# Performance work log

Measured on AMD Instinct MI355X. Metric: run time of the kernel, lower is better.

Reference implementation:

```python
import jax, jax.numpy as jnp
import numpy as np

N_NODES = 100000
N_EDGES = 1000000
N_GRAPHS = 64
NODE_IN = 4
HID = 64
SIG = 16
NEG_SLOPE = 0.2


def _gat_layer(x, src, dst, W, a_src, a_dst, bias, n_nodes, concat):
    # W: [H*D, F_in], a_src/a_dst: [H, D], bias: [H*D] or [D]
    H, D = a_src.shape
    h = (x @ W.T).reshape(-1, H, D)                      # [N, H, D]
    alpha_src = jnp.sum(h * a_src[None], axis=-1)        # [N, H]
    alpha_dst = jnp.sum(h * a_dst[None], axis=-1)        # [N, H]
    e = alpha_src[src] + alpha_dst[dst]                  # [E, H]
    e = jax.nn.leaky_relu(e, NEG_SLOPE)
    # segment softmax over edges grouped by destination node
    e_max = jax.ops.segment_max(e, dst, num_segments=n_nodes)   # [N, H]
    e_exp = jnp.exp(e - e_max[dst])                              # [E, H]
    denom = jax.ops.segment_sum(e_exp, dst, num_segments=n_nodes)
    alpha = e_exp / denom[dst]                                   # [E, H]
    out = jax.ops.segment_sum(alpha[:, :, None] * h[src], dst, num_segments=n_nodes)  # [N,H,D]
    if concat:
        out = out.reshape(-1, H * D)
    else:
        out = out.mean(axis=1)
    return out + bias


def setup_inputs() -> dict:
    key = jax.random.key(0)
    ks = jax.random.split(key, 16)
    x = jax.random.normal(ks[0], (N_NODES, NODE_IN), dtype=jnp.float32)
    edge_index = jax.random.randint(ks[1], (2, N_EDGES), 0, N_NODES, dtype=jnp.int32)
    batch = jnp.sort(jax.random.randint(ks[2], (N_NODES,), 0, N_GRAPHS, dtype=jnp.int32))
    s = 0.1
    # conv1: heads=2, concat -> out 128
    w1 = jax.random.normal(ks[3], (2 * HID, NODE_IN), dtype=jnp.float32) * s
    att_src1 = jax.random.normal(ks[4], (2, HID), dtype=jnp.float32) * s
    att_dst1 = jax.random.normal(ks[5], (2, HID), dtype=jnp.float32) * s
    b1 = jnp.zeros((2 * HID,), dtype=jnp.float32)
    # conv2: heads=1, mean -> out 64
    w2 = jax.random.normal(ks[6], (HID, 2 * HID), dtype=jnp.float32) * s
    att_src2 = jax.random.normal(ks[7], (1, HID), dtype=jnp.float32) * s
    att_dst2 = jax.random.normal(ks[8], (1, HID), dtype=jnp.float32) * s
    b2 = jnp.zeros((HID,), dtype=jnp.float32)
    wp = jax.random.normal(ks[9], (SIG, HID), dtype=jnp.float32) * s
    bp = jnp.zeros((SIG,), dtype=jnp.float32)
    return {"x": x, "edge_index": edge_index, "batch": batch,
            "w1": w1, "att_src1": att_src1, "att_dst1": att_dst1, "b1": b1,
            "w2": w2, "att_src2": att_src2, "att_dst2": att_dst2, "b2": b2,
            "wp": wp, "bp": bp}


def reference(x, edge_index, batch, w1, att_src1, att_dst1, b1,
              w2, att_src2, att_dst2, b2, wp, bp):
    n = x.shape[0]
    loops = jnp.arange(n, dtype=edge_index.dtype)
    src = jnp.concatenate([edge_index[0], loops])  # PyG GATConv adds self-loops
    dst = jnp.concatenate([edge_index[1], loops])
    h = jax.nn.elu(_gat_layer(x, src, dst, w1, att_src1, att_dst1, b1, n, concat=True))
    h = jax.nn.elu(_gat_layer(h, src, dst, w2, att_src2, att_dst2, b2, n, concat=False))
    # global mean pool by graph id
    sums = jax.ops.segment_sum(h, batch, num_segments=N_GRAPHS)
    cnts = jax.ops.segment_sum(jnp.ones((n,), h.dtype), batch, num_segments=N_GRAPHS)
    pooled = sums / jnp.maximum(cnts, 1.0)[:, None]
    return (pooled @ wp.T + bp).squeeze()
```

## Files before the change

### kernel.cpp

```cpp
#include <hip/hip_runtime.h>
#include <hip/hip_fp16.h>

#define N_NODES  100000
#define N_EDGES  1000000
#define E_TOT    1100000
#define E_CAP    1900000
#define N_GRAPHS 64

typedef _Float16 half8 __attribute__((ext_vector_type(8)));
typedef float    f32x4 __attribute__((ext_vector_type(4)));

__device__ __forceinline__ float elu_f(float v) {
    return v > 0.f ? v : expm1f(v);
}

__device__ __forceinline__ float lrelu(float v) {
    return v > 0.f ? v : 0.2f * v;
}

__global__ void k_pre(const float* __restrict__ w1,
                      const float* __restrict__ as1v, const float* __restrict__ ad1v,
                      const float* __restrict__ w2,
                      const float* __restrict__ as2v, const float* __restrict__ ad2v,
                      float* __restrict__ A1, float* __restrict__ D1,
                      float* __restrict__ B2, float* __restrict__ E2)
{
    int t = threadIdx.x;
    if (t < 128) {
        float acc = 0.f;
        for (int d = 0; d < 64; ++d) acc += w2[d * 128 + t] * as2v[d];
        B2[t] = acc;
    } else {
        int k = t - 128;
        float acc = 0.f;
        for (int d = 0; d < 64; ++d) acc += w2[d * 128 + k] * ad2v[d];
        E2[k] = acc;
    }
    if (t < 8) {
        int h = t >> 2, k = t & 3;
        float acc = 0.f;
        for (int d = 0; d < 64; ++d) acc += w1[(h * 64 + d) * 4 + k] * as1v[h * 64 + d];
        A1[t] = acc;
    } else if (t < 16) {
        int i = t - 8, h = i >> 2, k = i & 3;
        float acc = 0.f;
        for (int d = 0; d < 64; ++d) acc += w1[(h * 64 + d) * 4 + k] * ad1v[h * 64 + d];
        D1[i] = acc;
    }
}

__global__ void k_pre2(const float* __restrict__ w2, __half* __restrict__ w2frag)
{
    int f = blockIdx.x * 256 + threadIdx.x;
    int j = f & 7, ln = (f >> 3) & 63, g = f >> 9;
    int nt = g >> 2, ks = g & 3;
    int col = nt * 16 + (ln & 15);
    int k   = ks * 32 + ((ln >> 4) << 3) + j;
    w2frag[f] = __float2half(w2[col * 128 + k]);
}

__global__ void k_count(const int* __restrict__ ei, int* __restrict__ deg, int* __restrict__ pos)
{
    int e = blockIdx.x * blockDim.x + threadIdx.x;
    if (e >= E_TOT) return;
    int dst = (e < N_EDGES) ? ei[N_EDGES + e] : (e - N_EDGES);
    pos[e] = atomicAdd(&deg[dst], 1);
}

__global__ void k_scan1(const int* __restrict__ deg, int* __restrict__ rowptr, int* __restrict__ bsum)
{
    __shared__ int sh[256];
    int tid = threadIdx.x;
    int i = blockIdx.x * 256 + tid;
    int v = (i <= N_NODES) ? ((deg[i] + 7) & ~7) : 0;
    int acc = v;
    sh[tid] = acc; __syncthreads();
    for (int off = 1; off < 256; off <<= 1) {
        int add = (tid >= off) ? sh[tid - off] : 0;
        __syncthreads();
        acc += add;
        sh[tid] = acc;
        __syncthreads();
    }
    if (i <= N_NODES) rowptr[i] = acc - v;
    if (tid == 255) bsum[blockIdx.x] = acc;
}

__global__ void k_scan2(int* __restrict__ bsum, int nb)
{
    __shared__ int sh[512];
    int tid = threadIdx.x;
    int v = (tid < nb) ? bsum[tid] : 0;
    int acc = v;
    sh[tid] = acc; __syncthreads();
    for (int off = 1; off < 512; off <<= 1) {
        int add = (tid >= off) ? sh[tid - off] : 0;
        __syncthreads();
        acc += add;
        sh[tid] = acc;
        __syncthreads();
    }
    if (tid < nb) bsum[tid] = acc - v;
}

__global__ void k_scan3(int* __restrict__ rowptr, const int* __restrict__ bsum)
{
    int i = blockIdx.x * 256 + threadIdx.x;
    if (i <= N_NODES) rowptr[i] += bsum[blockIdx.x];
}

__global__ void k_scatter(const int* __restrict__ ei, const int* __restrict__ rowptr,
                          const int* __restrict__ pos, int* __restrict__ srcs)
{
    int e = blockIdx.x * blockDim.x + threadIdx.x;
    if (e >= E_TOT) return;
    int src = (e < N_EDGES) ? ei[e] : (e - N_EDGES);
    int dst = (e < N_EDGES) ? ei[N_EDGES + e] : (e - N_EDGES);
    srcs[rowptr[dst] + pos[e]] = src;
}

__global__ void __launch_bounds__(256) k_gather1x(
    const int* __restrict__ srcs, const int* __restrict__ rowptr, const int* __restrict__ deg,
    const float* __restrict__ x,
    const float* __restrict__ A1c, const float* __restrict__ D1c,
    float4* __restrict__ agg0, float4* __restrict__ agg1, float2* __restrict__ wsA)
{
    const int tid  = threadIdx.x;
    const int n    = blockIdx.x * 16 + (tid >> 4);
    const int lane = tid & 15;
    if (n >= N_NODES) return;

    const float4 A0 = ((const float4*)A1c)[0], A1v = ((const float4*)A1c)[1];
    const float4 D0 = ((const float4*)D1c)[0], D1v = ((const float4*)D1c)[1];
    const float4 xn = ((const float4*)x)[n];
    const float ad0 = xn.x * D0.x + xn.y * D0.y + xn.z * D0.z + xn.w * D0.w;
    const float ad1 = xn.x * D1v.x + xn.y * D1v.y + xn.z * D1v.z + xn.w * D1v.w;

    const int beg = rowptr[n], rend = beg + deg[n];
    float4 acc0 = {0.f, 0.f, 0.f, 0.f}, acc1 = {0.f, 0.f, 0.f, 0.f};
    float ws0 = 0.f, ws1 = 0.f;
    for (int j = beg + lane; j < rend; j += 16) {
        const int s = srcs[j];
        const float4 xs = ((const float4*)x)[s];
        const float as0 = xs.x * A0.x + xs.y * A0.y + xs.z * A0.z + xs.w * A0.w;
        const float as1 = xs.x * A1v.x + xs.y * A1v.y + xs.z * A1v.z + xs.w * A1v.w;
        const float w0 = __expf(lrelu(as0 + ad0));
        const float w1 = __expf(lrelu(as1 + ad1));
        acc0.x = fmaf(w0, xs.x, acc0.x); acc0.y = fmaf(w0, xs.y, acc0.y);
        acc0.z = fmaf(w0, xs.z, acc0.z); acc0.w = fmaf(w0, xs.w, acc0.w);
        acc1.x = fmaf(w1, xs.x, acc1.x); acc1.y = fmaf(w1, xs.y, acc1.y);
        acc1.z = fmaf(w1, xs.z, acc1.z); acc1.w = fmaf(w1, xs.w, acc1.w);
        ws0 += w0; ws1 += w1;
    }
    #pragma unroll
    for (int off = 1; off < 16; off <<= 1) {
        acc0.x += __shfl_xor(acc0.x, off, 64);
        acc0.y += __shfl_xor(acc0.y, off, 64);
        acc0.z += __shfl_xor(acc0.z, off, 64);
        acc0.w += __shfl_xor(acc0.w, off, 64);
        acc1.x += __shfl_xor(acc1.x, off, 64);
        acc1.y += __shfl_xor(acc1.y, off, 64);
        acc1.z += __shfl_xor(acc1.z, off, 64);
        acc1.w += __shfl_xor(acc1.w, off, 64);
        ws0    += __shfl_xor(ws0,    off, 64);
        ws1    += __shfl_xor(ws1,    off, 64);
    }
    if (lane == 0) {
        agg0[n] = acc0;
        agg1[n] = acc1;
        wsA[n]  = make_float2(ws0, ws1);
    }
}

#define H2_NPB 64
#define SROW_H_LD 136
__global__ void __launch_bounds__(256) k_h2f(
    const float4* __restrict__ agg0, const float4* __restrict__ agg1,
    const float2* __restrict__ wsA,
    const float* __restrict__ w1, const float* __restrict__ b1,
    const __half* __restrict__ w2frag,
    const float* __restrict__ B2, const float* __restrict__ E2,
    __half* __restrict__ h2h, float* __restrict__ as2, float* __restrict__ ad2)
{
    __shared__ __align__(16) _Float16 srow[H2_NPB * SROW_H_LD];
    const int tid = threadIdx.x;
    const int bn  = blockIdx.x * H2_NPB;

    #pragma unroll 4
    for (int t = 0; t < 16; ++t) {
        int i = tid + t * 256;
        int r = i >> 6, c2 = i & 63;
        int n = bn + r;
        int head = c2 >> 5;
        float4 a; float ws;
        if (n < N_NODES) {
            a = head ? agg1[n] : agg0[n];
            float2 w = wsA[n];
            ws = head ? w.y : w.x;
        } else { a = make_float4(0.f, 0.f, 0.f, 0.f); ws = 1.f; }
        const float4 wA = ((const float4*)w1)[2 * c2];
        const float4 wB = ((const float4*)w1)[2 * c2 + 1];
        const float2 bb = ((const float2*)b1)[c2];
        float inv = 1.f / ws;
        float v0 = elu_f((a.x * wA.x + a.y * wA.y + a.z * wA.z + a.w * wA.w) * inv + bb.x);
        float v1 = elu_f((a.x * wB.x + a.y * wB.y + a.z * wB.z + a.w * wB.w) * inv + bb.y);
        *(__half2*)&srow[r * SROW_H_LD + 2 * c2] = __floats2half2_rn(v0, v1);
    }
    __syncthreads();

    {
        int r = tid >> 2, q = tid & 3;
        const __half2* row = (const __half2*)&srow[r * SROW_H_LD];
        float ps = 0.f, pd = 0.f;
        #pragma unroll 4
        for (int i = 0; i < 16; ++i) {
            int c2 = q * 16 + i;
            float2 v  = __half22float2(row[c2]);
            float2 Bv = ((const float2*)B2)[c2];
            float2 Ev = ((const float2*)E2)[c2];
            ps += v.x * Bv.x + v.y * Bv.y;
            pd += v.x * Ev.x + v.y * Ev.y;
        }
        ps += __shfl_xor(ps, 1, 64); ps += __shfl_xor(ps, 2, 64);
        pd += __shfl_xor(pd, 1, 64); pd += __shfl_xor(pd, 2, 64);
        int n = bn + r;
        if (q == 0 && n < N_NODES) { as2[n] = ps; ad2[n] = pd; }
    }

    const int lane = tid & 63;
    const int wv   = tid >> 6;
    const int mrow = lane & 15;
    const int kc   = lane >> 4;
    f32x4 acc[4] = {{0.f,0.f,0.f,0.f},{0.f,0.f,0.f,0.f},{0.f,0.f,0.f,0.f},{0.f,0.f,0.f,0.f}};
    const half8* __restrict__ wf = (const half8*)w2frag;
    #pragma unroll
    for (int ks = 0; ks < 4; ++ks) {
        const half8 af = *(const half8*)&srow[(wv * 16 + mrow) * SROW_H_LD + ks * 32 + kc * 8];
        #pragma unroll
        for (int nt = 0; nt < 4; ++nt) {
            const half8 bf = wf[(nt * 4 + ks) * 64 + lane];
            acc[nt] = __builtin_amdgcn_mfma_f32_16x16x32_f16(af, bf, acc[nt], 0, 0, 0);
        }
    }
    #pragma unroll
    for (int nt = 0; nt < 4; ++nt) {
        #pragma unroll
        for (int reg = 0; reg < 4; ++reg) {
            int node = bn + wv * 16 + ((lane >> 4) << 2) + reg;
            int dim  = nt * 16 + (lane & 15);
            if (node < N_NODES) h2h[(size_t)node * 64 + dim] = __float2half(acc[nt][reg]);
        }
    }
}

__global__ void __launch_bounds__(256) k_weights2(
    const int* __restrict__ rowptr, const int* __restrict__ deg, int* __restrict__ srcs,
    const float* __restrict__ as2, const float* __restrict__ ad2,
    float* __restrict__ w0p)
{
    int n = blockIdx.x * 16 + (threadIdx.x >> 4);
    int lane = threadIdx.x & 15;
    if (n >= N_NODES) return;
    int beg = rowptr[n], pend = rowptr[n + 1], rend = beg + deg[n];
    float adv = ad2[n];
    for (int j = beg + lane; j < pend; j += 16) {
        if (j < rend) {
            w0p[j] = __expf(lrelu(as2[srcs[j]] + adv));
        } else {
            srcs[j] = 0;
            w0p[j] = 0.f;
        }
    }
}

__global__ void __launch_bounds__(256) k_gather2(
    const int* __restrict__ srcs, const int* __restrict__ rowptr,
    const float* __restrict__ wcsr, const _Float16* __restrict__ h2h,
    const float* __restrict__ b2, float* __restrict__ out2)
{
    const int tid  = threadIdx.x;
    const int n    = blockIdx.x * 4 + (tid >> 6);
    const int lane = tid & 63;
    const int eg   = lane >> 3;
    const int dq   = lane & 7;
    const int beg = rowptr[n], end = rowptr[n + 1];

    half8 hacc = {0, 0, 0, 0, 0, 0, 0, 0};
    float wsum = 0.f;
    for (int j = beg + eg; j < end; j += 8) {
        const int   s = srcs[j];
        const float w = wcsr[j];
        const half8 v = *(const half8*)&h2h[(size_t)s * 64 + dq * 8];
        const _Float16 wh = (_Float16)w;
        const half8 ws8 = {wh, wh, wh, wh, wh, wh, wh, wh};
        hacc += v * ws8;
        wsum += w;
    }
    float a0 = (float)hacc[0], a1 = (float)hacc[1], a2 = (float)hacc[2], a3 = (float)hacc[3];
    float a4 = (float)hacc[4], a5 = (float)hacc[5], a6 = (float)hacc[6], a7 = (float)hacc[7];
    #pragma unroll
    for (int off = 8; off < 64; off <<= 1) {
        a0 += __shfl_xor(a0, off, 64);
        a1 += __shfl_xor(a1, off, 64);
        a2 += __shfl_xor(a2, off, 64);
        a3 += __shfl_xor(a3, off, 64);
        a4 += __shfl_xor(a4, off, 64);
        a5 += __shfl_xor(a5, off, 64);
        a6 += __shfl_xor(a6, off, 64);
        a7 += __shfl_xor(a7, off, 64);
        wsum += __shfl_xor(wsum, off, 64);
    }
    if (eg == 0) {
        const float inv = 1.f / wsum;
        const float4 bA = ((const float4*)b2)[dq * 2];
        const float4 bB = ((const float4*)b2)[dq * 2 + 1];
        float4 oA, oB;
        oA.x = elu_f(a0 * inv + bA.x);
        oA.y = elu_f(a1 * inv + bA.y);
        oA.z = elu_f(a2 * inv + bA.z);
        oA.w = elu_f(a3 * inv + bA.w);
        oB.x = elu_f(a4 * inv + bB.x);
        oB.y = elu_f(a5 * inv + bB.y);
        oB.z = elu_f(a6 * inv + bB.z);
        oB.w = elu_f(a7 * inv + bB.w);
        float4* orow = (float4*)(out2 + (size_t)n * 64);
        orow[dq * 2]     = oA;
        orow[dq * 2 + 1] = oB;
    }
}

__global__ void __launch_bounds__(256) k_pool(
    const float* __restrict__ out2, const int* __restrict__ batch,
    float* __restrict__ pool, float* __restrict__ cnt)
{
    const int wv = threadIdx.x >> 6, d = threadIdx.x & 63;
    const int wid = blockIdx.x * 4 + wv;
    const int per = (N_NODES + 2047) / 2048;
    int n0 = wid * per, n1 = min(n0 + per, N_NODES);
    if (n0 >= n1) return;
    float acc = 0.f; int g = batch[n0]; int run = 0;
    for (int n = n0; n < n1; ++n) {
        int gn = batch[n];
        if (gn != g) {
            atomicAdd(&pool[g * 64 + d], acc);
            if (d == 0) atomicAdd(&cnt[g], (float)run);
            acc = 0.f; run = 0; g = gn;
        }
        acc += out2[(size_t)n * 64 + d];
        ++run;
    }
    atomicAdd(&pool[g * 64 + d], acc);
    if (d == 0) atomicAdd(&cnt[g], (float)run);
}

__global__ void k_head(const float* __restrict__ pool, const float* __restrict__ cnt,
                       const float* __restrict__ wp, const float* __restrict__ bp,
                       float* __restrict__ out)
{
    int t = threadIdx.x;
    int g = t >> 4, s = t & 15;
    float c = cnt[g]; if (c < 1.f) c = 1.f;
    float acc = bp[s];
    for (int d = 0; d < 64; ++d) acc += (pool[g * 64 + d] / c) * wp[s * 64 + d];
    out[g * 16 + s] = acc;
}

extern "C" void kernel_launch(void* const* d_in, const int* in_sizes, int n_in,
                              void* d_out, int out_size, void* d_ws, size_t ws_size,
                              hipStream_t stream)
{
    const float* x     = (const float*)d_in[0];
    const int*   ei    = (const int*)  d_in[1];
    const int*   batch = (const int*)  d_in[2];
    const float* w1    = (const float*)d_in[3];
    const float* asr1  = (const float*)d_in[4];
    const float* adr1  = (const float*)d_in[5];
    const float* b1    = (const float*)d_in[6];
    const float* w2    = (const float*)d_in[7];
    const float* asr2  = (const float*)d_in[8];
    const float* adr2  = (const float*)d_in[9];
    const float* b2    = (const float*)d_in[10];
    const float* wp    = (const float*)d_in[11];
    const float* bp    = (const float*)d_in[12];
    float* out = (float*)d_out;

    float4* agg0 = (float4*)d_ws;
    float4* agg1 = agg0 + N_NODES;
    float2* wsA  = (float2*)(agg1 + N_NODES);
    __half* h2h  = (__half*)(wsA + N_NODES);
    float* out2  = (float*)(h2h + (size_t)N_NODES * 64);
    float* as2   = out2 + (size_t)N_NODES * 64;
    float* ad2   = as2 + N_NODES;
    float* pool  = ad2 + N_NODES;
    float* cnt   = pool + N_GRAPHS * 64;
    int* deg     = (int*)(cnt + N_GRAPHS);
    int* rowptr  = deg + N_NODES + 1;
    int* pos     = rowptr + N_NODES + 1;
    int* srcs    = pos + E_TOT;
    float* wcsr  = (float*)(srcs + E_CAP);
    int* bsum    = (int*)(wcsr + E_CAP);
    float* A1    = (float*)(bsum + 512);
    float* D1    = A1 + 8;
    float* B2    = D1 + 8;
    float* E2    = B2 + 128;
    __half* w2frag = (__half*)(((uintptr_t)(E2 + 128) + 15) & ~(uintptr_t)15);

    hipMemsetAsync(deg, 0, (size_t)(N_NODES + 1) * sizeof(int), stream);
    hipMemsetAsync(pool, 0, (size_t)(N_GRAPHS * 64 + N_GRAPHS) * sizeof(float), stream);

    k_pre<<<1, 256, 0, stream>>>(w1, asr1, adr1, w2, asr2, adr2, A1, D1, B2, E2);
    k_pre2<<<32, 256, 0, stream>>>(w2, w2frag);

    const int eb  = (E_TOT + 255) / 256;
    const int nb1 = (N_NODES + 1 + 255) / 256;
    k_count<<<eb, 256, 0, stream>>>(ei, deg, pos);
    k_scan1<<<nb1, 256, 0, stream>>>(deg, rowptr, bsum);
    k_scan2<<<1, 512, 0, stream>>>(bsum, nb1);
    k_scan3<<<nb1, 256, 0, stream>>>(rowptr, bsum);
    k_scatter<<<eb, 256, 0, stream>>>(ei, rowptr, pos, srcs);

    const int gb = (N_NODES + 15) / 16;
    k_gather1x<<<gb, 256, 0, stream>>>(srcs, rowptr, deg, x, A1, D1, agg0, agg1, wsA);

    k_h2f<<<(N_NODES + H2_NPB - 1) / H2_NPB, 256, 0, stream>>>(
        agg0, agg1, wsA, w1, b1, w2frag, B2, E2, h2h, as2, ad2);

    k_weights2<<<gb, 256, 0, stream>>>(rowptr, deg, srcs, as2, ad2, wcsr);
    k_gather2<<<N_NODES / 4, 256, 0, stream>>>(srcs, rowptr, wcsr, (const _Float16*)h2h,
                                               b2, out2);

    k_pool<<<512, 256, 0, stream>>>(out2, batch, pool, cnt);
    k_head<<<1, 1024, 0, stream>>>(pool, cnt, wp, bp, out);
}
```

Before: 230.7 us.

## Merge precompute kernels, scatter via atomic cursor, split gather2 launch

Merges the two weight-precompute kernels into one 33-block launch. CSR construction no longer writes a per-edge position array in the count pass; the scan fills a per-node cursor and the scatter claims slots with atomics, which saves a 1.1M-int write and read but adds a second atomic pass and makes edge order within a row nondeterministic. The second-layer gather is split into two half-size launches over node ranges, which adds a launch without any evident benefit.

```diff
diff --git a/kernel.cpp b/kernel.cpp
--- a/kernel.cpp
+++ b/kernel.cpp
@@ -18,53 +18,53 @@
     return v > 0.f ? v : 0.2f * v;
 }
 
-__global__ void k_pre(const float* __restrict__ w1,
-                      const float* __restrict__ as1v, const float* __restrict__ ad1v,
-                      const float* __restrict__ w2,
-                      const float* __restrict__ as2v, const float* __restrict__ ad2v,
-                      float* __restrict__ A1, float* __restrict__ D1,
-                      float* __restrict__ B2, float* __restrict__ E2)
-{
-    int t = threadIdx.x;
-    if (t < 128) {
-        float acc = 0.f;
-        for (int d = 0; d < 64; ++d) acc += w2[d * 128 + t] * as2v[d];
-        B2[t] = acc;
+__global__ void k_preall(const float* __restrict__ w1,
+                         const float* __restrict__ as1v, const float* __restrict__ ad1v,
+                         const float* __restrict__ w2,
+                         const float* __restrict__ as2v, const float* __restrict__ ad2v,
+                         float* __restrict__ A1, float* __restrict__ D1,
+                         float* __restrict__ B2, float* __restrict__ E2,
+                         __half* __restrict__ w2frag)
+{
+    if (blockIdx.x == 0) {
+        int t = threadIdx.x;
+        if (t < 128) {
+            float acc = 0.f;
+            for (int d = 0; d < 64; ++d) acc += w2[d * 128 + t] * as2v[d];
+            B2[t] = acc;
+        } else {
+            int k = t - 128;
+            float acc = 0.f;
+            for (int d = 0; d < 64; ++d) acc += w2[d * 128 + k] * ad2v[d];
+            E2[k] = acc;
+        }
+        if (t < 8) {
+            int h = t >> 2, k = t & 3;
+            float acc = 0.f;
+            for (int d = 0; d < 64; ++d) acc += w1[(h * 64 + d) * 4 + k] * as1v[h * 64 + d];
+            A1[t] = acc;
+        } else if (t < 16) {
+            int i = t - 8, h = i >> 2, k = i & 3;
+            float acc = 0.f;
+            for (int d = 0; d < 64; ++d) acc += w1[(h * 64 + d) * 4 + k] * ad1v[h * 64 + d];
+            D1[i] = acc;
+        }
     } else {
-        int k = t - 128;
-        float acc = 0.f;
-        for (int d = 0; d < 64; ++d) acc += w2[d * 128 + k] * ad2v[d];
-        E2[k] = acc;
-    }
-    if (t < 8) {
-        int h = t >> 2, k = t & 3;
-        float acc = 0.f;
-        for (int d = 0; d < 64; ++d) acc += w1[(h * 64 + d) * 4 + k] * as1v[h * 64 + d];
-        A1[t] = acc;
-    } else if (t < 16) {
-        int i = t - 8, h = i >> 2, k = i & 3;
-        float acc = 0.f;
-        for (int d = 0; d < 64; ++d) acc += w1[(h * 64 + d) * 4 + k] * ad1v[h * 64 + d];
-        D1[i] = acc;
-    }
-}
-
-__global__ void k_pre2(const float* __restrict__ w2, __half* __restrict__ w2frag)
-{
-    int f = blockIdx.x * 256 + threadIdx.x;
-    int j = f & 7, ln = (f >> 3) & 63, g = f >> 9;
-    int nt = g >> 2, ks = g & 3;
-    int col = nt * 16 + (ln & 15);
-    int k   = ks * 32 + ((ln >> 4) << 3) + j;
-    w2frag[f] = __float2half(w2[col * 128 + k]);
-}
-
-__global__ void k_count(const int* __restrict__ ei, int* __restrict__ deg, int* __restrict__ pos)
+        int f = (blockIdx.x - 1) * 256 + threadIdx.x;
+        int j = f & 7, ln = (f >> 3) & 63, g = f >> 9;
+        int nt = g >> 2, ks = g & 3;
+        int col = nt * 16 + (ln & 15);
+        int k   = ks * 32 + ((ln >> 4) << 3) + j;
+        w2frag[f] = __float2half(w2[col * 128 + k]);
+    }
+}
+
+__global__ void k_count(const int* __restrict__ ei, int* __restrict__ deg)
 {
     int e = blockIdx.x * blockDim.x + threadIdx.x;
     if (e >= E_TOT) return;
     int dst = (e < N_EDGES) ? ei[N_EDGES + e] : (e - N_EDGES);
-    pos[e] = atomicAdd(&deg[dst], 1);
+    atomicAdd(&deg[dst], 1);
 }
 
 __global__ void k_scan1(const int* __restrict__ deg, int* __restrict__ rowptr, int* __restrict__ bsum)
@@ -103,20 +103,25 @@
     if (tid < nb) bsum[tid] = acc - v;
 }
 
-__global__ void k_scan3(int* __restrict__ rowptr, const int* __restrict__ bsum)
+__global__ void k_scan3(int* __restrict__ rowptr, int* __restrict__ cur, const int* __restrict__ bsum)
 {
     int i = blockIdx.x * 256 + threadIdx.x;
-    if (i <= N_NODES) rowptr[i] += bsum[blockIdx.x];
-}
-
-__global__ void k_scatter(const int* __restrict__ ei, const int* __restrict__ rowptr,
-                          const int* __restrict__ pos, int* __restrict__ srcs)
+    if (i <= N_NODES) {
+        int v = rowptr[i] + bsum[blockIdx.x];
+        rowptr[i] = v;
+        if (i < N_NODES) cur[i] = v;
+    }
+}
+
+__global__ void k_scatter(const int* __restrict__ ei, int* __restrict__ cur,
+                          int* __restrict__ srcs)
 {
     int e = blockIdx.x * blockDim.x + threadIdx.x;
     if (e >= E_TOT) return;
     int src = (e < N_EDGES) ? ei[e] : (e - N_EDGES);
     int dst = (e < N_EDGES) ? ei[N_EDGES + e] : (e - N_EDGES);
-    srcs[rowptr[dst] + pos[e]] = src;
+    int j = atomicAdd(&cur[dst], 1);
+    srcs[j] = src;
 }
 
 __global__ void __launch_bounds__(256) k_gather1x(
@@ -276,10 +281,10 @@
 __global__ void __launch_bounds__(256) k_gather2(
     const int* __restrict__ srcs, const int* __restrict__ rowptr,
     const float* __restrict__ wcsr, const _Float16* __restrict__ h2h,
-    const float* __restrict__ b2, float* __restrict__ out2)
+    const float* __restrict__ b2, float* __restrict__ out2, int nbase)
 {
     const int tid  = threadIdx.x;
-    const int n    = blockIdx.x * 4 + (tid >> 6);
+    const int n    = nbase + blockIdx.x * 4 + (tid >> 6);
     const int lane = tid & 63;
     const int eg   = lane >> 3;
     const int dq   = lane & 7;
@@ -395,8 +400,8 @@
     float* cnt   = pool + N_GRAPHS * 64;
     int* deg     = (int*)(cnt + N_GRAPHS);
     int* rowptr  = deg + N_NODES + 1;
-    int* pos     = rowptr + N_NODES + 1;
-    int* srcs    = pos + E_TOT;
+    int* cur     = rowptr + N_NODES + 1;
+    int* srcs    = cur + N_NODES;
     float* wcsr  = (float*)(srcs + E_CAP);
     int* bsum    = (int*)(wcsr + E_CAP);
     float* A1    = (float*)(bsum + 512);
@@ -408,16 +413,15 @@
     hipMemsetAsync(deg, 0, (size_t)(N_NODES + 1) * sizeof(int), stream);
     hipMemsetAsync(pool, 0, (size_t)(N_GRAPHS * 64 + N_GRAPHS) * sizeof(float), stream);
 
-    k_pre<<<1, 256, 0, stream>>>(w1, asr1, adr1, w2, asr2, adr2, A1, D1, B2, E2);
-    k_pre2<<<32, 256, 0, stream>>>(w2, w2frag);
+    k_preall<<<33, 256, 0, stream>>>(w1, asr1, adr1, w2, asr2, adr2, A1, D1, B2, E2, w2frag);
 
     const int eb  = (E_TOT + 255) / 256;
     const int nb1 = (N_NODES + 1 + 255) / 256;
-    k_count<<<eb, 256, 0, stream>>>(ei, deg, pos);
+    k_count<<<eb, 256, 0, stream>>>(ei, deg);
     k_scan1<<<nb1, 256, 0, stream>>>(deg, rowptr, bsum);
     k_scan2<<<1, 512, 0, stream>>>(bsum, nb1);
-    k_scan3<<<nb1, 256, 0, stream>>>(rowptr, bsum);
-    k_scatter<<<eb, 256, 0, stream>>>(ei, rowptr, pos, srcs);
+    k_scan3<<<nb1, 256, 0, stream>>>(rowptr, cur, bsum);
+    k_scatter<<<eb, 256, 0, stream>>>(ei, cur, srcs);
 
     const int gb = (N_NODES + 15) / 16;
     k_gather1x<<<gb, 256, 0, stream>>>(srcs, rowptr, deg, x, A1, D1, agg0, agg1, wsA);
@@ -426,8 +430,10 @@
         agg0, agg1, wsA, w1, b1, w2frag, B2, E2, h2h, as2, ad2);
 
     k_weights2<<<gb, 256, 0, stream>>>(rowptr, deg, srcs, as2, ad2, wcsr);
-    k_gather2<<<N_NODES / 4, 256, 0, stream>>>(srcs, rowptr, wcsr, (const _Float16*)h2h,
-                                               b2, out2);
+    k_gather2<<<N_NODES / 8, 256, 0, stream>>>(srcs, rowptr, wcsr, (const _Float16*)h2h,
+                                               b2, out2, 0);
+    k_gather2<<<N_NODES / 8, 256, 0, stream>>>(srcs, rowptr, wcsr, (const _Float16*)h2h,
+                                               b2, out2, N_NODES / 2);
 
     k_pool<<<512, 256, 0, stream>>>(out2, batch, pool, cnt);
     k_head<<<1, 1024, 0, stream>>>(pool, cnt, wp, bp, out);
```

New measurement: 290.5 us. +25.9%, slower.
